# Kernel optimization log

Hardware: AMD Instinct MI355X
Metric: run time of the kernel (lower is better)

## Reference

```python
import jax, jax.numpy as jnp
import numpy as np

# ---- model constants (match init_kwargs) ----
NX, NY, H, K, GRID = 32, 1, 64, 3, 5
MID = 2 * H + 1            # 129, middle width of each KAN block
NB = GRID + K              # 8 B-spline basis functions per edge
BATCH = 65536


def _grid_pts():
    # uniform extended grid on [-1, 1] with K extra knots each side: GRID+2K+1 pts
    step = 2.0 / GRID
    return jnp.arange(-K, GRID + K + 1, dtype=jnp.float32) * step - 1.0


def bspline_basis(x):
    """Cox-de Boor B-spline bases. x: [B, I] -> [B, I, GRID+K]."""
    g = _grid_pts()[None, None, :]          # [1,1,P]
    xe = x[..., None]                       # [B,I,1]
    B0 = ((xe >= g[..., :-1]) & (xe < g[..., 1:])).astype(x.dtype)
    Bp = B0
    for p in range(1, K + 1):
        left = (xe - g[..., :-(p + 1)]) / (g[..., p:-1] - g[..., :-(p + 1)])
        right = (g[..., p + 1:] - xe) / (g[..., p + 1:] - g[..., 1:-p])
        Bp = left * Bp[..., :-1] + right * Bp[..., 1:]
    return Bp  # [B, I, NB]


def kan_layer(x, coef, sb, ss, bias):
    """pykan KANLayer: y_o = sum_i sb[i,o]*silu(x_i) + ss[i,o]*spline_io(x_i) + bias_o.
    x: [B,I]; coef: [I,O,NB]; sb, ss: [I,O]; bias: [O]."""
    bs = bspline_basis(x)                                   # [B,I,NB]
    spline = jnp.einsum('bip,iop->bo', bs, coef * ss[:, :, None])
    return jax.nn.silu(x) @ sb + spline + bias


def setup_inputs() -> dict:
    key = jax.random.key(0)
    ks = iter(jax.random.split(key, 40))

    def xavier(k, shape, fan_in, fan_out):
        gain = np.sqrt(2.0)  # relu gain, as in the torch module
        std = gain * np.sqrt(2.0 / (fan_in + fan_out))
        return (std * jax.random.normal(k, shape, dtype=jnp.float32))

    inp = {
        'x': jax.random.normal(next(ks), (BATCH, NX), dtype=jnp.float32),
        'W_in': xavier(next(ks), (NX, H), NX, H),
        'b_in': jnp.zeros((H,), jnp.float32),
        'W_out': xavier(next(ks), (H, NY), H, NY),
    }
    for l in range(2):  # num_hidden_layers KAN blocks, each = 2 KANLayers
        for tag, (din, dout) in [('a', (H, MID)), ('b', (MID, H))]:
            inp[f'coef{l}{tag}'] = xavier(next(ks), (din, dout, NB), din * NB, dout)
            inp[f'sb{l}{tag}'] = xavier(next(ks), (din, dout), din, dout)
            inp[f'ss{l}{tag}'] = jnp.ones((din, dout), jnp.float32)
            inp[f'bias{l}{tag}'] = jnp.zeros((dout,), jnp.float32)
    return inp


def reference(x, W_in, b_in, W_out,
              coef0a, sb0a, ss0a, bias0a, coef0b, sb0b, ss0b, bias0b,
              coef1a, sb1a, ss1a, bias1a, coef1b, sb1b, ss1b, bias1b):
    h = jax.nn.relu(x @ W_in + b_in)
    for (ca, sa, ta, ba, cb, sbb, tb, bb) in (
        (coef0a, sb0a, ss0a, bias0a, coef0b, sb0b, ss0b, bias0b),
        (coef1a, sb1a, ss1a, bias1a, coef1b, sb1b, ss1b, bias1b),
    ):
        h = kan_layer(h, ca, sa, ta, ba)   # H -> 2H+1
        h = kan_layer(h, cb, sbb, tb, bb)  # 2H+1 -> H
    return jax.nn.sigmoid(h @ W_out)       # [B, NY]
```

## Files before the change

kernel.cpp:

```cpp
#include <hip/hip_runtime.h>
#include <math.h>
#include <stdint.h>

#define BATCH 65536
#define TB 128

typedef __fp16   fp16x2  __attribute__((ext_vector_type(2)));
typedef _Float16 half8   __attribute__((ext_vector_type(8)));
typedef float    floatx16 __attribute__((ext_vector_type(16)));

#define SH 68
#define SM 130
#define HM_SLICE (32*SM + 64)

#define WIN 2048
#define KSA 36
#define KSB 74
#define WA (KSA*5*512)
#define WB (KSB*2*512)
#define WTOT (WIN + 2*(WA+WB))

__global__ void setup_weights(
    const float* __restrict__ W_in,
    const float* __restrict__ c0a, const float* __restrict__ sb0a, const float* __restrict__ ss0a,
    const float* __restrict__ c0b, const float* __restrict__ sb0b, const float* __restrict__ ss0b,
    const float* __restrict__ c1a, const float* __restrict__ sb1a, const float* __restrict__ ss1a,
    const float* __restrict__ c1b, const float* __restrict__ sb1b, const float* __restrict__ ss1b,
    _Float16* __restrict__ wt) {
  int idx = blockIdx.x * 256 + threadIdx.x;
  if (idx >= WTOT) return;
  float v = 0.0f;
  if (idx < WIN) {
    int ks = idx >> 10; int nt = (idx >> 9) & 1;
    int q = idx & 511;  int l = q >> 3;   int j = q & 7;
    int n = nt*32 + (l & 31);
    int k = ks*16 + (l >> 5)*8 + j;
    v = W_in[k*64 + n];
  } else {
    int e2   = idx - WIN;
    int pair = (e2 >= WA + WB) ? 1 : 0;
    int e    = e2 - pair * (WA + WB);
    if (e < WA) {
      const float* coef = pair ? c1a : c0a;
      const float* sb   = pair ? sb1a : sb0a;
      const float* ss   = pair ? ss1a : ss0a;
      int ks = e / 2560; int r = e - ks*2560;
      int nt = r >> 9;   int q = r & 511;
      int l  = q >> 3;   int j = q & 7;
      int n  = nt*32 + (l & 31);
      int k  = ks*16 + (l >> 5)*8 + j;
      if (n < 129) {
        if (k < 512) { int i = k >> 3, p = k & 7; v = ss[i*129+n] * coef[(i*129+n)*8 + p]; }
        else         { int i = k - 512; if (i < 64) v = sb[i*129+n]; }
      }
    } else {
      const float* coef = pair ? c1b : c0b;
      const float* sb   = pair ? sb1b : sb0b;
      const float* ss   = pair ? ss1b : ss0b;
      int eb = e - WA;
      int ks = eb >> 10; int r = eb & 1023;
      int nt = r >> 9;   int q = r & 511;
      int l  = q >> 3;   int j = q & 7;
      int n  = nt*32 + (l & 31);
      int k  = ks*16 + (l >> 5)*8 + j;
      if (k < 1032)      { int i = k >> 3, p = k & 7; v = ss[i*64+n] * coef[(i*64+n)*8 + p]; }
      else if (k >= 1040){ int s = k - 1040; if (s < 129) v = sb[s*64+n]; }
    }
  }
  wt[idx] = (_Float16)v;
}

__device__ __forceinline__ half8 feat8(float x) {
  float s  = fmaf(x, 2.5f, 5.5f);
  float mf = floorf(s);
  int   m  = (int)mf;
  float u  = s - mf;
  float t  = 1.0f - u;
  float u2 = u*u;
  float t2 = t*t;
  float w0 = t2 * (t * (1.0f/6.0f));
  float w3 = u2 * (u * (1.0f/6.0f));
  float w1 = fmaf(u2, fmaf(0.5f, u, -1.0f), 2.0f/3.0f);
  float w2 = fmaf(t2, fmaf(0.5f, t, -1.0f), 2.0f/3.0f);
  union { fp16x2 h2[2]; uint64_t u64; } P;
  P.h2[0] = __builtin_amdgcn_cvt_pkrtz(w0, w1);
  P.h2[1] = __builtin_amdgcn_cvt_pkrtz(w2, w3);
  uint64_t T = ((unsigned)m <= 10u) ? P.u64 : 0ull;
  int A = (m << 4) - 48;
  uint64_t L  = T << (A & 63);
  uint64_t R_ = T >> ((-A) & 63);
  uint64_t q0 = (A >= 0) ? ((A < 64) ? L : 0ull) : R_;
  uint64_t q1 = (A >= 64) ? L : ((A > 0) ? R_ : 0ull);
  union { uint64_t q[2]; half8 h; } R;
  R.q[0] = q0; R.q[1] = q1;
  return R.h;
}

__device__ __forceinline__ float extract_half(uint32_t w, int khs) {
  union { uint32_t u; _Float16 h[2]; } cv;
  cv.u = w >> khs;
  return (float)cv.h[0];
}

__device__ __forceinline__ float silu(float x) {
  return x * __builtin_amdgcn_rcpf(1.0f + __expf(-x));
}

template<int KSPL, int KSIL, int NT, int SIN, int O, int SOUT>
__device__ __forceinline__ void kan_layer(
    const _Float16* __restrict__ hinw, _Float16* __restrict__ houtw,
    const _Float16* __restrict__ wt, const float* __restrict__ bias, int lane) {
  constexpr int KTOT = KSPL + KSIL;
  constexpr int NG   = KSPL / 8;
  constexpr int KR   = KSPL - NG*8;
  static_assert(KR == 0 || KR == 1, "remainder must be 0/1");
  const int ln  = lane & 31;
  const int kh  = lane >> 5;
  const int khs = kh << 4;
  const half8* __restrict__ bp = (const half8*)wt + lane;
  floatx16 acc[NT];
  #pragma unroll
  for (int j = 0; j < NT; ++j)
    #pragma unroll
    for (int e = 0; e < 16; ++e) acc[j][e] = 0.0f;

  half8 B[2][NT];
  #pragma unroll
  for (int d = 0; d < 2; ++d)
    #pragma unroll
    for (int j = 0; j < NT; ++j) B[d][j] = bp[(d*NT + j)*64];

  union H8 { half8 h; uint32_t d[4]; };

  #pragma unroll 1
  for (int g = 0; g < NG; ++g) {
    H8 ha, hb;
    ha.h = *(const half8*)&hinw[ln*SIN + g*16];
    hb.h = *(const half8*)&hinw[ln*SIN + g*16 + 8];
    #pragma unroll
    for (int u = 0; u < 8; ++u) {
      uint32_t w = (u < 4) ? ha.d[u] : hb.d[u & 3];
      half8 A = feat8(extract_half(w, khs));
      #pragma unroll
      for (int j = 0; j < NT; ++j)
        acc[j] = __builtin_amdgcn_mfma_f32_32x32x16_f16(A, B[u & 1][j], acc[j], 0, 0, 0);
      #pragma unroll
      for (int j = 0; j < NT; ++j)
        B[u & 1][j] = bp[((g*8 + u + 2)*NT + j)*64];
    }
  }

  if (KR == 1) {
    constexpr int ks = NG*8;
    H8 hc;
    hc.h = *(const half8*)&hinw[ln*SIN + ks*2];
    half8 A = feat8(extract_half(hc.d[0], khs));
    #pragma unroll
    for (int j = 0; j < NT; ++j)
      acc[j] = __builtin_amdgcn_mfma_f32_32x32x16_f16(A, B[ks & 1][j], acc[j], 0, 0, 0);
    #pragma unroll
    for (int j = 0; j < NT; ++j)
      B[ks & 1][j] = bp[((ks + 2)*NT + j)*64];
  }

  #pragma unroll
  for (int sk = 0; sk < KSIL; ++sk) {
    const int ks = KSPL + sk;
    half8 h8 = *(const half8*)&hinw[ln*SIN + sk*16 + kh*8];
    union { fp16x2 h2[4]; half8 v; } Au;
    #pragma unroll
    for (int e = 0; e < 4; ++e) {
      float s0 = silu((float)h8[2*e]);
      float s1 = silu((float)h8[2*e + 1]);
      Au.h2[e] = __builtin_amdgcn_cvt_pkrtz(s0, s1);
    }
    #pragma unroll
    for (int j = 0; j < NT; ++j)
      acc[j] = __builtin_amdgcn_mfma_f32_32x32x16_f16(Au.v, B[ks & 1][j], acc[j], 0, 0, 0);
    const int nks = (ks + 2 < KTOT) ? (ks + 2) : (KTOT - 1);
    #pragma unroll
    for (int j = 0; j < NT; ++j)
      B[ks & 1][j] = bp[(nks*NT + j)*64];
  }

  #pragma unroll
  for (int j = 0; j < NT; ++j) {
    int col = j*32 + ln;
    if (col < O) {
      float bv = bias[col];
      #pragma unroll
      for (int r = 0; r < 16; ++r) {
        int row = (r & 3) + 8*(r >> 2) + 4*kh;
        houtw[row*SOUT + col] = (_Float16)(acc[j][r] + bv);
      }
    }
  }
}

extern "C" __global__ void __launch_bounds__(256, 2)
kan_forward(const float* __restrict__ x, const float* __restrict__ b_in,
            const float* __restrict__ W_out, const _Float16* __restrict__ wt,
            const float* __restrict__ bias0a, const float* __restrict__ bias0b,
            const float* __restrict__ bias1a, const float* __restrict__ bias1b,
            float* __restrict__ out) {
  __shared__ _Float16 hM[4][HM_SLICE];
  __shared__ _Float16 hH[4][32*SH];
  const int t    = threadIdx.x;
  const int wv   = t >> 6;
  const int lane = t & 63;
  const int ln   = lane & 31;
  const int kh   = lane >> 5;
  _Float16* hMw = hM[wv];
  _Float16* hHw = hH[wv];
  const int rbase = blockIdx.x * TB + wv * 32;

  hMw[32*SM + lane] = (_Float16)0.0f;
  if (lane < 32) hMw[lane*SM + 129] = (_Float16)0.0f;

  {
    const float* xr = &x[(rbase + ln)*32 + kh*8];
    float4 v0 = *(const float4*)&xr[0];
    float4 v1 = *(const float4*)&xr[4];
    float4 v2 = *(const float4*)&xr[16];
    float4 v3 = *(const float4*)&xr[20];
    union { fp16x2 h2[4]; half8 h8; } A0, A1;
    A0.h2[0] = __builtin_amdgcn_cvt_pkrtz(v0.x, v0.y);
    A0.h2[1] = __builtin_amdgcn_cvt_pkrtz(v0.z, v0.w);
    A0.h2[2] = __builtin_amdgcn_cvt_pkrtz(v1.x, v1.y);
    A0.h2[3] = __builtin_amdgcn_cvt_pkrtz(v1.z, v1.w);
    A1.h2[0] = __builtin_amdgcn_cvt_pkrtz(v2.x, v2.y);
    A1.h2[1] = __builtin_amdgcn_cvt_pkrtz(v2.z, v2.w);
    A1.h2[2] = __builtin_amdgcn_cvt_pkrtz(v3.x, v3.y);
    A1.h2[3] = __builtin_amdgcn_cvt_pkrtz(v3.z, v3.w);
    const half8* bp = (const half8*)wt + lane;
    #pragma unroll
    for (int nt = 0; nt < 2; ++nt) {
      floatx16 a;
      #pragma unroll
      for (int e = 0; e < 16; ++e) a[e] = 0.0f;
      a = __builtin_amdgcn_mfma_f32_32x32x16_f16(A0.h8, bp[nt*64],       a, 0, 0, 0);
      a = __builtin_amdgcn_mfma_f32_32x32x16_f16(A1.h8, bp[(2 + nt)*64], a, 0, 0, 0);
      int col = nt*32 + ln;
      float bv = b_in[col];
      #pragma unroll
      for (int r = 0; r < 16; ++r) {
        int row = (r & 3) + 8*(r >> 2) + 4*kh;
        hHw[row*SH + col] = (_Float16)fmaxf(a[r] + bv, 0.0f);
      }
    }
  }

  kan_layer<32,4,5,SH,129,SM>(hHw, hMw, wt + WIN,             bias0a, lane);
  kan_layer<65,9,2,SM, 64,SH>(hMw, hHw, wt + WIN + WA,        bias0b, lane);
  kan_layer<32,4,5,SH,129,SM>(hHw, hMw, wt + WIN + WA + WB,   bias1a, lane);
  kan_layer<65,9,2,SM, 64,SH>(hMw, hHw, wt + WIN + 2*WA + WB, bias1b, lane);

  {
    float s = 0.0f;
    #pragma unroll
    for (int j = 0; j < 32; ++j)
      s = fmaf((float)hHw[ln*SH + kh*32 + j], W_out[kh*32 + j], s);
    s += __shfl_down(s, 32);
    if (lane < 32)
      out[rbase + ln] = __builtin_amdgcn_rcpf(1.0f + __expf(-s));
  }
}

extern "C" void kernel_launch(void* const* d_in, const int* in_sizes, int n_in,
                              void* d_out, int out_size, void* d_ws, size_t ws_size,
                              hipStream_t stream) {
  const float* x     = (const float*)d_in[0];
  const float* W_in  = (const float*)d_in[1];
  const float* b_in  = (const float*)d_in[2];
  const float* W_out = (const float*)d_in[3];
  const float* c0a = (const float*)d_in[4];  const float* sb0a = (const float*)d_in[5];
  const float* ss0a= (const float*)d_in[6];  const float* bias0a=(const float*)d_in[7];
  const float* c0b = (const float*)d_in[8];  const float* sb0b = (const float*)d_in[9];
  const float* ss0b= (const float*)d_in[10]; const float* bias0b=(const float*)d_in[11];
  const float* c1a = (const float*)d_in[12]; const float* sb1a = (const float*)d_in[13];
  const float* ss1a= (const float*)d_in[14]; const float* bias1a=(const float*)d_in[15];
  const float* c1b = (const float*)d_in[16]; const float* sb1b = (const float*)d_in[17];
  const float* ss1b= (const float*)d_in[18]; const float* bias1b=(const float*)d_in[19];
  float*    out = (float*)d_out;
  _Float16* wt  = (_Float16*)d_ws;

  setup_weights<<<(WTOT + 255)/256, 256, 0, stream>>>(
      W_in, c0a, sb0a, ss0a, c0b, sb0b, ss0b,
      c1a, sb1a, ss1a, c1b, sb1b, ss1b, wt);

  kan_forward<<<BATCH/TB, 256, 0, stream>>>(
      x, b_in, W_out, wt, bias0a, bias0b, bias1a, bias1b, out);
}
```

Baseline: 155.0 us.

## Stage KAN weights into shared LDS via cooperative async DMA with triple buffering

Instead of every wave loading its own copy of the B-operand weights straight from global memory into registers, the four waves now cooperatively DMA each weight chunk into shared memory with global_load_lds, using a three-slot ring and barriers. This aims to cut redundant global/L2 traffic by a factor of the wave count and to hide load latency behind MFMA work. The staging buffer reuses the other layer's activation LDS region, which adds block-wide barriers per chunk and couples the waves' progress. Biases are also preloaded into registers up front.

```diff
diff --git a/kernel.cpp b/kernel.cpp
--- a/kernel.cpp
+++ b/kernel.cpp
@@ -6,6 +6,7 @@
 #define TB 128
 
 typedef __fp16   fp16x2  __attribute__((ext_vector_type(2)));
+typedef _Float16 half4   __attribute__((ext_vector_type(4)));
 typedef _Float16 half8   __attribute__((ext_vector_type(8)));
 typedef float    floatx16 __attribute__((ext_vector_type(16)));
 
@@ -70,6 +71,36 @@
   wt[idx] = (_Float16)v;
 }
 
+__device__ __forceinline__ void dma16(const void* g, void* l) {
+  __builtin_amdgcn_global_load_lds(
+      (const __attribute__((address_space(1))) void*)g,
+      (__attribute__((address_space(3))) void*)l,
+      16, 0, 0);
+}
+
+template<int NL>
+__device__ __forceinline__ void dma_chunk(const _Float16* gsrc, _Float16* ldst,
+                                          int lane, int wv) {
+  const char* g = (const char*)gsrc + lane*16;
+  char* l = (char*)ldst;
+  #pragma unroll
+  for (int L = 0; L < NL; ++L)
+    if ((L & 3) == wv) dma16(g + L*1024, l + L*1024);
+}
+
+template<int N>
+__device__ __forceinline__ void waitv() {
+  if constexpr (N == 0)      asm volatile("s_waitcnt vmcnt(0)" ::: "memory");
+  else if constexpr (N == 1) asm volatile("s_waitcnt vmcnt(1)" ::: "memory");
+  else                       asm volatile("s_waitcnt vmcnt(2)" ::: "memory");
+}
+
+__device__ __forceinline__ void bar() {
+  asm volatile("" ::: "memory");
+  __builtin_amdgcn_s_barrier();
+  asm volatile("" ::: "memory");
+}
+
 __device__ __forceinline__ half8 feat8(float x) {
   float s  = fmaf(x, 2.5f, 5.5f);
   float mf = floorf(s);
@@ -109,64 +140,69 @@
 template<int KSPL, int KSIL, int NT, int SIN, int O, int SOUT>
 __device__ __forceinline__ void kan_layer(
     const _Float16* __restrict__ hinw, _Float16* __restrict__ houtw,
-    const _Float16* __restrict__ wt, const float* __restrict__ bias, int lane) {
-  constexpr int KTOT = KSPL + KSIL;
-  constexpr int NG   = KSPL / 8;
-  constexpr int KR   = KSPL - NG*8;
-  static_assert(KR == 0 || KR == 1, "remainder must be 0/1");
+    _Float16* __restrict__ stg, const _Float16* __restrict__ wtl,
+    const float* __restrict__ bv, int lane, int wv) {
+  constexpr int CTOT = (KSPL + KSIL) / 2;
+  constexpr int NPS  = KSPL / 2;
+  constexpr int MIX  = KSPL & 1;
+  constexpr int NPSI = (KSIL - MIX) / 2;
+  constexpr int CH   = NT * 1024;
+  constexpr int NL   = NT * 2;
+  constexpr int W    = (NL >= 8) ? 2 : 1;
+  static_assert(NPS + MIX + NPSI == CTOT, "chunk accounting");
   const int ln  = lane & 31;
   const int kh  = lane >> 5;
   const int khs = kh << 4;
-  const half8* __restrict__ bp = (const half8*)wt + lane;
+
   floatx16 acc[NT];
   #pragma unroll
   for (int j = 0; j < NT; ++j)
     #pragma unroll
     for (int e = 0; e < 16; ++e) acc[j][e] = 0.0f;
 
-  half8 B[2][NT];
-  #pragma unroll
-  for (int d = 0; d < 2; ++d)
-    #pragma unroll
-    for (int j = 0; j < NT; ++j) B[d][j] = bp[(d*NT + j)*64];
-
-  union H8 { half8 h; uint32_t d[4]; };
+  dma_chunk<NL>(wtl,      stg,      lane, wv);
+  dma_chunk<NL>(wtl + CH, stg + CH, lane, wv);
 
   #pragma unroll 1
-  for (int g = 0; g < NG; ++g) {
-    H8 ha, hb;
-    ha.h = *(const half8*)&hinw[ln*SIN + g*16];
-    hb.h = *(const half8*)&hinw[ln*SIN + g*16 + 8];
-    #pragma unroll
-    for (int u = 0; u < 8; ++u) {
-      uint32_t w = (u < 4) ? ha.d[u] : hb.d[u & 3];
-      half8 A = feat8(extract_half(w, khs));
-      #pragma unroll
-      for (int j = 0; j < NT; ++j)
-        acc[j] = __builtin_amdgcn_mfma_f32_32x32x16_f16(A, B[u & 1][j], acc[j], 0, 0, 0);
-      #pragma unroll
-      for (int j = 0; j < NT; ++j)
-        B[u & 1][j] = bp[((g*8 + u + 2)*NT + j)*64];
-    }
-  }
-
-  if (KR == 1) {
-    constexpr int ks = NG*8;
-    H8 hc;
-    hc.h = *(const half8*)&hinw[ln*SIN + ks*2];
-    half8 A = feat8(extract_half(hc.d[0], khs));
+  for (int c = 0; c < NPS; ++c) {
+    waitv<W>();
+    bar();
+    dma_chunk<NL>(wtl + (c+2)*CH, stg + ((c+2)%3)*CH, lane, wv);
+    const half8* bp = (const half8*)(stg + (c%3)*CH) + lane;
+    half8 b0[NT], b1[NT];
+    #pragma unroll
+    for (int j = 0; j < NT; ++j) b0[j] = bp[j*64];
+    #pragma unroll
+    for (int j = 0; j < NT; ++j) b1[j] = bp[(NT + j)*64];
+    union { half4 v; uint32_t d[2]; } hq;
+    hq.v = *(const half4*)&hinw[ln*SIN + 4*c];
+    half8 A0 = feat8(extract_half(hq.d[0], khs));
+    half8 A1 = feat8(extract_half(hq.d[1], khs));
     #pragma unroll
     for (int j = 0; j < NT; ++j)
-      acc[j] = __builtin_amdgcn_mfma_f32_32x32x16_f16(A, B[ks & 1][j], acc[j], 0, 0, 0);
+      acc[j] = __builtin_amdgcn_mfma_f32_32x32x16_f16(A0, b0[j], acc[j], 0, 0, 0);
     #pragma unroll
     for (int j = 0; j < NT; ++j)
-      B[ks & 1][j] = bp[((ks + 2)*NT + j)*64];
-  }
-
-  #pragma unroll
-  for (int sk = 0; sk < KSIL; ++sk) {
-    const int ks = KSPL + sk;
-    half8 h8 = *(const half8*)&hinw[ln*SIN + sk*16 + kh*8];
+      acc[j] = __builtin_amdgcn_mfma_f32_32x32x16_f16(A1, b1[j], acc[j], 0, 0, 0);
+  }
+
+  if constexpr (MIX) {
+    constexpr int c = NPS;
+    waitv<W>();
+    bar();
+    if constexpr (c + 2 < CTOT)
+      dma_chunk<NL>(wtl + (c+2)*CH, stg + ((c+2)%3)*CH, lane, wv);
+    const half8* bp = (const half8*)(stg + (c%3)*CH) + lane;
+    half8 b0[NT], b1[NT];
+    #pragma unroll
+    for (int j = 0; j < NT; ++j) b0[j] = bp[j*64];
+    #pragma unroll
+    for (int j = 0; j < NT; ++j) b1[j] = bp[(NT + j)*64];
+    half8 A0 = feat8((float)hinw[ln*SIN + 2*(KSPL-1) + kh]);
+    #pragma unroll
+    for (int j = 0; j < NT; ++j)
+      acc[j] = __builtin_amdgcn_mfma_f32_32x32x16_f16(A0, b0[j], acc[j], 0, 0, 0);
+    half8 h8 = *(const half8*)&hinw[ln*SIN + kh*8];
     union { fp16x2 h2[4]; half8 v; } Au;
     #pragma unroll
     for (int e = 0; e < 4; ++e) {
@@ -176,22 +212,50 @@
     }
     #pragma unroll
     for (int j = 0; j < NT; ++j)
-      acc[j] = __builtin_amdgcn_mfma_f32_32x32x16_f16(Au.v, B[ks & 1][j], acc[j], 0, 0, 0);
-    const int nks = (ks + 2 < KTOT) ? (ks + 2) : (KTOT - 1);
-    #pragma unroll
-    for (int j = 0; j < NT; ++j)
-      B[ks & 1][j] = bp[(nks*NT + j)*64];
-  }
+      acc[j] = __builtin_amdgcn_mfma_f32_32x32x16_f16(Au.v, b1[j], acc[j], 0, 0, 0);
+  }
+
+  #pragma unroll
+  for (int i = 0; i < NPSI; ++i) {
+    const int c = NPS + MIX + i;
+    if (c == CTOT - 1) waitv<0>(); else waitv<W>();
+    bar();
+    if (c + 2 < CTOT)
+      dma_chunk<NL>(wtl + (c+2)*CH, stg + ((c+2)%3)*CH, lane, wv);
+    const half8* bp = (const half8*)(stg + (c%3)*CH) + lane;
+    half8 bb[2][NT];
+    #pragma unroll
+    for (int j = 0; j < NT; ++j) bb[0][j] = bp[j*64];
+    #pragma unroll
+    for (int j = 0; j < NT; ++j) bb[1][j] = bp[(NT + j)*64];
+    #pragma unroll
+    for (int kl = 0; kl < 2; ++kl) {
+      const int sk = MIX + 2*i + kl;
+      half8 h8 = *(const half8*)&hinw[ln*SIN + sk*16 + kh*8];
+      union { fp16x2 h2[4]; half8 v; } Au;
+      #pragma unroll
+      for (int e = 0; e < 4; ++e) {
+        float s0 = silu((float)h8[2*e]);
+        float s1 = silu((float)h8[2*e + 1]);
+        Au.h2[e] = __builtin_amdgcn_cvt_pkrtz(s0, s1);
+      }
+      #pragma unroll
+      for (int j = 0; j < NT; ++j)
+        acc[j] = __builtin_amdgcn_mfma_f32_32x32x16_f16(Au.v, bb[kl][j], acc[j], 0, 0, 0);
+    }
+  }
+
+  bar();
 
   #pragma unroll
   for (int j = 0; j < NT; ++j) {
     int col = j*32 + ln;
     if (col < O) {
-      float bv = bias[col];
+      float b = bv[j];
       #pragma unroll
       for (int r = 0; r < 16; ++r) {
         int row = (r & 3) + 8*(r >> 2) + 4*kh;
-        houtw[row*SOUT + col] = (_Float16)(acc[j][r] + bv);
+        houtw[row*SOUT + col] = (_Float16)(acc[j][r] + b);
       }
     }
   }
@@ -203,8 +267,8 @@
             const float* __restrict__ bias0a, const float* __restrict__ bias0b,
             const float* __restrict__ bias1a, const float* __restrict__ bias1b,
             float* __restrict__ out) {
-  __shared__ _Float16 hM[4][HM_SLICE];
-  __shared__ _Float16 hH[4][32*SH];
+  __shared__ __align__(16) _Float16 hM[4][HM_SLICE];
+  __shared__ __align__(16) _Float16 hH[4][32*SH];
   const int t    = threadIdx.x;
   const int wv   = t >> 6;
   const int lane = t & 63;
@@ -212,13 +276,30 @@
   const int kh   = lane >> 5;
   _Float16* hMw = hM[wv];
   _Float16* hHw = hH[wv];
+  _Float16* stM = &hM[0][0];
+  _Float16* stH = &hH[0][0];
   const int rbase = blockIdx.x * TB + wv * 32;
 
-  hMw[32*SM + lane] = (_Float16)0.0f;
-  if (lane < 32) hMw[lane*SM + 129] = (_Float16)0.0f;
+  if (wv == 3) {
+    hMw[32*SM + lane] = (_Float16)0.0f;
+    if (lane >= 20 && lane < 32) hMw[lane*SM + 129] = (_Float16)0.0f;
+  }
+
+  float bA0[5], bA1[5], bB0[2], bB1[2], bi[2];
+  #pragma unroll
+  for (int j = 0; j < 5; ++j) {
+    int col = j*32 + ln; int cc = (col < 129) ? col : 0;
+    bA0[j] = bias0a[cc]; bA1[j] = bias1a[cc];
+  }
+  #pragma unroll
+  for (int j = 0; j < 2; ++j) {
+    int col = j*32 + ln;
+    bB0[j] = bias0b[col]; bB1[j] = bias1b[col]; bi[j] = b_in[col];
+  }
 
   {
-    const float* xr = &x[(rbase + ln)*32 + kh*8];
+    dma_chunk<4>(wt, stM, lane, wv);
+    const float* xr = &x[(size_t)(rbase + ln)*32 + kh*8];
     float4 v0 = *(const float4*)&xr[0];
     float4 v1 = *(const float4*)&xr[4];
     float4 v2 = *(const float4*)&xr[16];
@@ -232,7 +313,9 @@
     A1.h2[1] = __builtin_amdgcn_cvt_pkrtz(v2.z, v2.w);
     A1.h2[2] = __builtin_amdgcn_cvt_pkrtz(v3.x, v3.y);
     A1.h2[3] = __builtin_amdgcn_cvt_pkrtz(v3.z, v3.w);
-    const half8* bp = (const half8*)wt + lane;
+    waitv<0>();
+    bar();
+    const half8* bp = (const half8*)stM + lane;
     #pragma unroll
     for (int nt = 0; nt < 2; ++nt) {
       floatx16 a;
@@ -241,7 +324,7 @@
       a = __builtin_amdgcn_mfma_f32_32x32x16_f16(A0.h8, bp[nt*64],       a, 0, 0, 0);
       a = __builtin_amdgcn_mfma_f32_32x32x16_f16(A1.h8, bp[(2 + nt)*64], a, 0, 0, 0);
       int col = nt*32 + ln;
-      float bv = b_in[col];
+      float bv = bi[nt];
       #pragma unroll
       for (int r = 0; r < 16; ++r) {
         int row = (r & 3) + 8*(r >> 2) + 4*kh;
@@ -249,11 +332,12 @@
       }
     }
   }
-
-  kan_layer<32,4,5,SH,129,SM>(hHw, hMw, wt + WIN,             bias0a, lane);
-  kan_layer<65,9,2,SM, 64,SH>(hMw, hHw, wt + WIN + WA,        bias0b, lane);
-  kan_layer<32,4,5,SH,129,SM>(hHw, hMw, wt + WIN + WA + WB,   bias1a, lane);
-  kan_layer<65,9,2,SM, 64,SH>(hMw, hHw, wt + WIN + 2*WA + WB, bias1b, lane);
+  bar();
+
+  kan_layer<32,4,5,SH,129,SM>(hHw, hMw, stM, wt + WIN,             bA0, lane, wv);
+  kan_layer<65,9,2,SM, 64,SH>(hMw, hHw, stH, wt + WIN + WA,        bB0, lane, wv);
+  kan_layer<32,4,5,SH,129,SM>(hHw, hMw, stM, wt + WIN + WA + WB,   bA1, lane, wv);
+  kan_layer<65,9,2,SM, 64,SH>(hMw, hHw, stH, wt + WIN + 2*WA + WB, bB1, lane, wv);
 
   {
     float s = 0.0f;
```

New measurement: 169.7 us. 1.09x slower.

## Switch KAN MFMA tiling from 32x32x16 to 16x16x32 with 16-row wave tiles

Applied to the files above, without the earlier changes.

Each wave now processes 16 batch rows instead of 32, using 16x16x32 fp16 MFMA instructions with a new packed weight layout (32-wide K steps, 16-wide N tiles). The block tile drops to 64 rows and launch bounds allow 4 blocks per CU, aiming for higher occupancy and fewer wasted padded columns. The wide layer-a path (9 N tiles) loads B fragments per step instead of double-buffering them, to limit register pressure. The weight setup kernel now writes 8 halves per thread. The risk is that each weight fragment is reused across only 16 rows, so weight traffic per row doubles.

```diff
diff --git a/kernel.cpp b/kernel.cpp
--- a/kernel.cpp
+++ b/kernel.cpp
@@ -3,21 +3,20 @@
 #include <stdint.h>
 
 #define BATCH 65536
-#define TB 128
+#define TB 64
 
 typedef __fp16   fp16x2  __attribute__((ext_vector_type(2)));
 typedef _Float16 half8   __attribute__((ext_vector_type(8)));
-typedef float    floatx16 __attribute__((ext_vector_type(16)));
+typedef float    floatx4 __attribute__((ext_vector_type(4)));
 
 #define SH 68
-#define SM 130
-#define HM_SLICE (32*SM + 64)
+#define SM 168
 
 #define WIN 2048
-#define KSA 36
-#define KSB 74
-#define WA (KSA*5*512)
-#define WB (KSB*2*512)
+#define KSA 18
+#define KSB 38
+#define WA (KSA*9*512)
+#define WB (KSB*4*512)
 #define WTOT (WIN + 2*(WA+WB))
 
 __global__ void setup_weights(
@@ -27,47 +26,71 @@
     const float* __restrict__ c1a, const float* __restrict__ sb1a, const float* __restrict__ ss1a,
     const float* __restrict__ c1b, const float* __restrict__ sb1b, const float* __restrict__ ss1b,
     _Float16* __restrict__ wt) {
-  int idx = blockIdx.x * 256 + threadIdx.x;
-  if (idx >= WTOT) return;
-  float v = 0.0f;
-  if (idx < WIN) {
-    int ks = idx >> 10; int nt = (idx >> 9) & 1;
-    int q = idx & 511;  int l = q >> 3;   int j = q & 7;
-    int n = nt*32 + (l & 31);
-    int k = ks*16 + (l >> 5)*8 + j;
-    v = W_in[k*64 + n];
+  int e = (blockIdx.x * 256 + threadIdx.x) * 8;
+  if (e >= WTOT) return;
+  float v[8];
+  #pragma unroll
+  for (int j = 0; j < 8; ++j) v[j] = 0.0f;
+
+  if (e < WIN) {
+    int nt = e >> 9;
+    int l  = (e >> 3) & 63;
+    int n  = nt*16 + (l & 15);
+    int kb = (l >> 4) * 8;
+    #pragma unroll
+    for (int j = 0; j < 8; ++j) v[j] = W_in[(kb + j)*64 + n];
   } else {
-    int e2   = idx - WIN;
+    int e2   = e - WIN;
     int pair = (e2 >= WA + WB) ? 1 : 0;
-    int e    = e2 - pair * (WA + WB);
-    if (e < WA) {
+    int e3   = e2 - pair * (WA + WB);
+    if (e3 < WA) {
       const float* coef = pair ? c1a : c0a;
       const float* sb   = pair ? sb1a : sb0a;
       const float* ss   = pair ? ss1a : ss0a;
-      int ks = e / 2560; int r = e - ks*2560;
-      int nt = r >> 9;   int q = r & 511;
-      int l  = q >> 3;   int j = q & 7;
-      int n  = nt*32 + (l & 31);
-      int k  = ks*16 + (l >> 5)*8 + j;
+      int ks = e3 / 4608; int r = e3 - ks*4608;
+      int nt = r >> 9;    int l = (r >> 3) & 63;
+      int n  = nt*16 + (l & 15);
+      int kb = ks*32 + (l >> 4)*8;
       if (n < 129) {
-        if (k < 512) { int i = k >> 3, p = k & 7; v = ss[i*129+n] * coef[(i*129+n)*8 + p]; }
-        else         { int i = k - 512; if (i < 64) v = sb[i*129+n]; }
+        if (kb < 512) {
+          int i = kb >> 3;
+          float s = ss[i*129 + n];
+          const float* cp = &coef[(i*129 + n)*8];
+          #pragma unroll
+          for (int j = 0; j < 8; ++j) v[j] = s * cp[j];
+        } else {
+          #pragma unroll
+          for (int j = 0; j < 8; ++j) v[j] = sb[(kb - 512 + j)*129 + n];
+        }
       }
     } else {
       const float* coef = pair ? c1b : c0b;
       const float* sb   = pair ? sb1b : sb0b;
       const float* ss   = pair ? ss1b : ss0b;
-      int eb = e - WA;
-      int ks = eb >> 10; int r = eb & 1023;
-      int nt = r >> 9;   int q = r & 511;
-      int l  = q >> 3;   int j = q & 7;
-      int n  = nt*32 + (l & 31);
-      int k  = ks*16 + (l >> 5)*8 + j;
-      if (k < 1032)      { int i = k >> 3, p = k & 7; v = ss[i*64+n] * coef[(i*64+n)*8 + p]; }
-      else if (k >= 1040){ int s = k - 1040; if (s < 129) v = sb[s*64+n]; }
-    }
-  }
-  wt[idx] = (_Float16)v;
+      int e4 = e3 - WA;
+      int ks = e4 >> 11;  int r = e4 & 2047;
+      int nt = r >> 9;    int l = (r >> 3) & 63;
+      int n  = nt*16 + (l & 15);
+      int kb = ks*32 + (l >> 4)*8;
+      if (kb < 1032) {
+        int i = kb >> 3;
+        float s = ss[i*64 + n];
+        const float* cp = &coef[(i*64 + n)*8];
+        #pragma unroll
+        for (int j = 0; j < 8; ++j) v[j] = s * cp[j];
+      } else if (kb >= 1056) {
+        #pragma unroll
+        for (int j = 0; j < 8; ++j) {
+          int si = kb - 1056 + j;
+          if (si < 129) v[j] = sb[si*64 + n];
+        }
+      }
+    }
+  }
+  half8 h;
+  #pragma unroll
+  for (int j = 0; j < 8; ++j) h[j] = (_Float16)v[j];
+  *(half8*)&wt[e] = h;
 }
 
 __device__ __forceinline__ half8 feat8(float x) {
@@ -96,173 +119,183 @@
   return R.h;
 }
 
-__device__ __forceinline__ float extract_half(uint32_t w, int khs) {
-  union { uint32_t u; _Float16 h[2]; } cv;
-  cv.u = w >> khs;
-  return (float)cv.h[0];
-}
-
 __device__ __forceinline__ float silu(float x) {
   return x * __builtin_amdgcn_rcpf(1.0f + __expf(-x));
 }
 
 template<int KSPL, int KSIL, int NT, int SIN, int O, int SOUT>
-__device__ __forceinline__ void kan_layer(
+__device__ __forceinline__ void kan_layer16(
     const _Float16* __restrict__ hinw, _Float16* __restrict__ houtw,
-    const _Float16* __restrict__ wt, const float* __restrict__ bias, int lane) {
+    const _Float16* __restrict__ wtl, const float* __restrict__ bias, int lane) {
   constexpr int KTOT = KSPL + KSIL;
   constexpr int NG   = KSPL / 8;
   constexpr int KR   = KSPL - NG*8;
   static_assert(KR == 0 || KR == 1, "remainder must be 0/1");
-  const int ln  = lane & 31;
-  const int kh  = lane >> 5;
-  const int khs = kh << 4;
-  const half8* __restrict__ bp = (const half8*)wt + lane;
-  floatx16 acc[NT];
+  const int ln16 = lane & 15;
+  const int kg   = lane >> 4;
+  const half8* __restrict__ bp = (const half8*)wtl + lane;
+  floatx4 acc[NT];
   #pragma unroll
   for (int j = 0; j < NT; ++j)
     #pragma unroll
-    for (int e = 0; e < 16; ++e) acc[j][e] = 0.0f;
-
-  half8 B[2][NT];
-  #pragma unroll
-  for (int d = 0; d < 2; ++d)
-    #pragma unroll
-    for (int j = 0; j < NT; ++j) B[d][j] = bp[(d*NT + j)*64];
-
-  union H8 { half8 h; uint32_t d[4]; };
-
-  #pragma unroll 1
-  for (int g = 0; g < NG; ++g) {
-    H8 ha, hb;
-    ha.h = *(const half8*)&hinw[ln*SIN + g*16];
-    hb.h = *(const half8*)&hinw[ln*SIN + g*16 + 8];
-    #pragma unroll
-    for (int u = 0; u < 8; ++u) {
-      uint32_t w = (u < 4) ? ha.d[u] : hb.d[u & 3];
-      half8 A = feat8(extract_half(w, khs));
-      #pragma unroll
-      for (int j = 0; j < NT; ++j)
-        acc[j] = __builtin_amdgcn_mfma_f32_32x32x16_f16(A, B[u & 1][j], acc[j], 0, 0, 0);
-      #pragma unroll
-      for (int j = 0; j < NT; ++j)
-        B[u & 1][j] = bp[((g*8 + u + 2)*NT + j)*64];
-    }
-  }
-
-  if (KR == 1) {
-    constexpr int ks = NG*8;
-    H8 hc;
-    hc.h = *(const half8*)&hinw[ln*SIN + ks*2];
-    half8 A = feat8(extract_half(hc.d[0], khs));
-    #pragma unroll
-    for (int j = 0; j < NT; ++j)
-      acc[j] = __builtin_amdgcn_mfma_f32_32x32x16_f16(A, B[ks & 1][j], acc[j], 0, 0, 0);
-    #pragma unroll
-    for (int j = 0; j < NT; ++j)
-      B[ks & 1][j] = bp[((ks + 2)*NT + j)*64];
-  }
-
-  #pragma unroll
-  for (int sk = 0; sk < KSIL; ++sk) {
-    const int ks = KSPL + sk;
-    half8 h8 = *(const half8*)&hinw[ln*SIN + sk*16 + kh*8];
-    union { fp16x2 h2[4]; half8 v; } Au;
-    #pragma unroll
-    for (int e = 0; e < 4; ++e) {
-      float s0 = silu((float)h8[2*e]);
-      float s1 = silu((float)h8[2*e + 1]);
-      Au.h2[e] = __builtin_amdgcn_cvt_pkrtz(s0, s1);
-    }
-    #pragma unroll
-    for (int j = 0; j < NT; ++j)
-      acc[j] = __builtin_amdgcn_mfma_f32_32x32x16_f16(Au.v, B[ks & 1][j], acc[j], 0, 0, 0);
-    const int nks = (ks + 2 < KTOT) ? (ks + 2) : (KTOT - 1);
-    #pragma unroll
-    for (int j = 0; j < NT; ++j)
-      B[ks & 1][j] = bp[(nks*NT + j)*64];
+    for (int el = 0; el < 4; ++el) acc[j][el] = 0.0f;
+
+  if constexpr (NT <= 4) {
+    half8 B[2][NT];
+    #pragma unroll
+    for (int d = 0; d < 2; ++d)
+      #pragma unroll
+      for (int j = 0; j < NT; ++j) B[d][j] = bp[(d*NT + j)*64];
+
+    #pragma unroll 1
+    for (int g = 0; g < NG; ++g) {
+      #pragma unroll
+      for (int u = 0; u < 8; ++u) {
+        const int ks = g*8 + u;
+        half8 A = feat8((float)hinw[ln16*SIN + ks*4 + kg]);
+        #pragma unroll
+        for (int j = 0; j < NT; ++j)
+          acc[j] = __builtin_amdgcn_mfma_f32_16x16x32_f16(A, B[u & 1][j], acc[j], 0, 0, 0);
+        #pragma unroll
+        for (int j = 0; j < NT; ++j)
+          B[u & 1][j] = bp[((ks + 2)*NT + j)*64];
+      }
+    }
+    if constexpr (KR == 1) {
+      constexpr int ks = NG*8;
+      half8 A = feat8((float)hinw[ln16*SIN + ks*4 + kg]);
+      #pragma unroll
+      for (int j = 0; j < NT; ++j)
+        acc[j] = __builtin_amdgcn_mfma_f32_16x16x32_f16(A, B[ks & 1][j], acc[j], 0, 0, 0);
+      #pragma unroll
+      for (int j = 0; j < NT; ++j)
+        B[ks & 1][j] = bp[((ks + 2)*NT + j)*64];
+    }
+    #pragma unroll
+    for (int sk = 0; sk < KSIL; ++sk) {
+      const int ks = KSPL + sk;
+      half8 h8 = *(const half8*)&hinw[ln16*SIN + sk*32 + kg*8];
+      union { fp16x2 h2[4]; half8 v; } Au;
+      #pragma unroll
+      for (int el = 0; el < 4; ++el) {
+        float s0 = silu((float)h8[2*el]);
+        float s1 = silu((float)h8[2*el + 1]);
+        Au.h2[el] = __builtin_amdgcn_cvt_pkrtz(s0, s1);
+      }
+      #pragma unroll
+      for (int j = 0; j < NT; ++j)
+        acc[j] = __builtin_amdgcn_mfma_f32_16x16x32_f16(Au.v, B[ks & 1][j], acc[j], 0, 0, 0);
+      const int nks = (ks + 2 < KTOT) ? (ks + 2) : (KTOT - 1);
+      #pragma unroll
+      for (int j = 0; j < NT; ++j)
+        B[ks & 1][j] = bp[(nks*NT + j)*64];
+    }
+  } else {
+    #pragma unroll 1
+    for (int g = 0; g < NG; ++g) {
+      #pragma unroll
+      for (int u = 0; u < 8; ++u) {
+        const int ks = g*8 + u;
+        half8 b[NT];
+        #pragma unroll
+        for (int j = 0; j < NT; ++j) b[j] = bp[(ks*NT + j)*64];
+        half8 A = feat8((float)hinw[ln16*SIN + ks*4 + kg]);
+        #pragma unroll
+        for (int j = 0; j < NT; ++j)
+          acc[j] = __builtin_amdgcn_mfma_f32_16x16x32_f16(A, b[j], acc[j], 0, 0, 0);
+      }
+    }
+    static_assert(KR == 0 || NT <= 4, "layer-a has no remainder");
+    #pragma unroll
+    for (int sk = 0; sk < KSIL; ++sk) {
+      const int ks = KSPL + sk;
+      half8 b[NT];
+      #pragma unroll
+      for (int j = 0; j < NT; ++j) b[j] = bp[(ks*NT + j)*64];
+      half8 h8 = *(const half8*)&hinw[ln16*SIN + sk*32 + kg*8];
+      union { fp16x2 h2[4]; half8 v; } Au;
+      #pragma unroll
+      for (int el = 0; el < 4; ++el) {
+        float s0 = silu((float)h8[2*el]);
+        float s1 = silu((float)h8[2*el + 1]);
+        Au.h2[el] = __builtin_amdgcn_cvt_pkrtz(s0, s1);
+      }
+      #pragma unroll
+      for (int j = 0; j < NT; ++j)
+        acc[j] = __builtin_amdgcn_mfma_f32_16x16x32_f16(Au.v, b[j], acc[j], 0, 0, 0);
+    }
   }
 
   #pragma unroll
   for (int j = 0; j < NT; ++j) {
-    int col = j*32 + ln;
+    int col = j*16 + ln16;
     if (col < O) {
       float bv = bias[col];
       #pragma unroll
-      for (int r = 0; r < 16; ++r) {
-        int row = (r & 3) + 8*(r >> 2) + 4*kh;
-        houtw[row*SOUT + col] = (_Float16)(acc[j][r] + bv);
-      }
-    }
-  }
-}
-
-extern "C" __global__ void __launch_bounds__(256, 2)
+      for (int r = 0; r < 4; ++r)
+        houtw[(kg*4 + r)*SOUT + col] = (_Float16)(acc[j][r] + bv);
+    }
+  }
+}
+
+extern "C" __global__ void __launch_bounds__(256, 4)
 kan_forward(const float* __restrict__ x, const float* __restrict__ b_in,
             const float* __restrict__ W_out, const _Float16* __restrict__ wt,
             const float* __restrict__ bias0a, const float* __restrict__ bias0b,
             const float* __restrict__ bias1a, const float* __restrict__ bias1b,
             float* __restrict__ out) {
-  __shared__ _Float16 hM[4][HM_SLICE];
-  __shared__ _Float16 hH[4][32*SH];
+  __shared__ _Float16 hM[4][16*SM];
+  __shared__ _Float16 hH[4][16*SH];
   const int t    = threadIdx.x;
   const int wv   = t >> 6;
   const int lane = t & 63;
-  const int ln   = lane & 31;
-  const int kh   = lane >> 5;
+  const int ln16 = lane & 15;
+  const int kg   = lane >> 4;
   _Float16* hMw = hM[wv];
   _Float16* hHw = hH[wv];
-  const int rbase = blockIdx.x * TB + wv * 32;
-
-  hMw[32*SM + lane] = (_Float16)0.0f;
-  if (lane < 32) hMw[lane*SM + 129] = (_Float16)0.0f;
+  const int rbase = blockIdx.x * TB + wv * 16;
+
+  #pragma unroll
+  for (int r = 0; r < 16; ++r) hMw[r*SM + 104 + lane] = (_Float16)0.0f;
 
   {
-    const float* xr = &x[(rbase + ln)*32 + kh*8];
+    const float* xr = &x[(size_t)(rbase + ln16)*32 + kg*8];
     float4 v0 = *(const float4*)&xr[0];
     float4 v1 = *(const float4*)&xr[4];
-    float4 v2 = *(const float4*)&xr[16];
-    float4 v3 = *(const float4*)&xr[20];
-    union { fp16x2 h2[4]; half8 h8; } A0, A1;
-    A0.h2[0] = __builtin_amdgcn_cvt_pkrtz(v0.x, v0.y);
-    A0.h2[1] = __builtin_amdgcn_cvt_pkrtz(v0.z, v0.w);
-    A0.h2[2] = __builtin_amdgcn_cvt_pkrtz(v1.x, v1.y);
-    A0.h2[3] = __builtin_amdgcn_cvt_pkrtz(v1.z, v1.w);
-    A1.h2[0] = __builtin_amdgcn_cvt_pkrtz(v2.x, v2.y);
-    A1.h2[1] = __builtin_amdgcn_cvt_pkrtz(v2.z, v2.w);
-    A1.h2[2] = __builtin_amdgcn_cvt_pkrtz(v3.x, v3.y);
-    A1.h2[3] = __builtin_amdgcn_cvt_pkrtz(v3.z, v3.w);
+    union { fp16x2 h2[4]; half8 h8; } A;
+    A.h2[0] = __builtin_amdgcn_cvt_pkrtz(v0.x, v0.y);
+    A.h2[1] = __builtin_amdgcn_cvt_pkrtz(v0.z, v0.w);
+    A.h2[2] = __builtin_amdgcn_cvt_pkrtz(v1.x, v1.y);
+    A.h2[3] = __builtin_amdgcn_cvt_pkrtz(v1.z, v1.w);
     const half8* bp = (const half8*)wt + lane;
     #pragma unroll
-    for (int nt = 0; nt < 2; ++nt) {
-      floatx16 a;
-      #pragma unroll
-      for (int e = 0; e < 16; ++e) a[e] = 0.0f;
-      a = __builtin_amdgcn_mfma_f32_32x32x16_f16(A0.h8, bp[nt*64],       a, 0, 0, 0);
-      a = __builtin_amdgcn_mfma_f32_32x32x16_f16(A1.h8, bp[(2 + nt)*64], a, 0, 0, 0);
-      int col = nt*32 + ln;
+    for (int nt = 0; nt < 4; ++nt) {
+      floatx4 a;
+      #pragma unroll
+      for (int el = 0; el < 4; ++el) a[el] = 0.0f;
+      a = __builtin_amdgcn_mfma_f32_16x16x32_f16(A.h8, bp[nt*64], a, 0, 0, 0);
+      int col = nt*16 + ln16;
       float bv = b_in[col];
       #pragma unroll
-      for (int r = 0; r < 16; ++r) {
-        int row = (r & 3) + 8*(r >> 2) + 4*kh;
-        hHw[row*SH + col] = (_Float16)fmaxf(a[r] + bv, 0.0f);
-      }
-    }
-  }
-
-  kan_layer<32,4,5,SH,129,SM>(hHw, hMw, wt + WIN,             bias0a, lane);
-  kan_layer<65,9,2,SM, 64,SH>(hMw, hHw, wt + WIN + WA,        bias0b, lane);
-  kan_layer<32,4,5,SH,129,SM>(hHw, hMw, wt + WIN + WA + WB,   bias1a, lane);
-  kan_layer<65,9,2,SM, 64,SH>(hMw, hHw, wt + WIN + 2*WA + WB, bias1b, lane);
+      for (int r = 0; r < 4; ++r)
+        hHw[(kg*4 + r)*SH + col] = (_Float16)fmaxf(a[r] + bv, 0.0f);
+    }
+  }
+
+  kan_layer16<16,2,9,SH,129,SM>(hHw, hMw, wt + WIN,             bias0a, lane);
+  kan_layer16<33,5,4,SM, 64,SH>(hMw, hHw, wt + WIN + WA,        bias0b, lane);
+  kan_layer16<16,2,9,SH,129,SM>(hHw, hMw, wt + WIN + WA + WB,   bias1a, lane);
+  kan_layer16<33,5,4,SM, 64,SH>(hMw, hHw, wt + WIN + 2*WA + WB, bias1b, lane);
 
   {
     float s = 0.0f;
     #pragma unroll
-    for (int j = 0; j < 32; ++j)
-      s = fmaf((float)hHw[ln*SH + kh*32 + j], W_out[kh*32 + j], s);
-    s += __shfl_down(s, 32);
-    if (lane < 32)
-      out[rbase + ln] = __builtin_amdgcn_rcpf(1.0f + __expf(-s));
+    for (int j = 0; j < 16; ++j)
+      s = fmaf((float)hHw[ln16*SH + kg*16 + j], W_out[kg*16 + j], s);
+    s += __shfl_xor(s, 16);
+    s += __shfl_xor(s, 32);
+    if (lane < 16)
+      out[rbase + ln16] = __builtin_amdgcn_rcpf(1.0f + __expf(-s));
   }
 }
 
@@ -284,7 +317,7 @@
   float*    out = (float*)d_out;
   _Float16* wt  = (_Float16*)d_ws;
 
-  setup_weights<<<(WTOT + 255)/256, 256, 0, stream>>>(
+  setup_weights<<<(WTOT/8 + 255)/256, 256, 0, stream>>>(
       W_in, c0a, sb0a, ss0a, c0b, sb0b, ss0b,
       c1a, sb1a, ss1a, c1b, sb1b, ss1b, wt);
 
```

New measurement: 175.7 us. 13.4% more time.

## Split each KAN layer's K dimension across wave pairs with LDS reduction

Applied to the files above, without the earlier changes.

Each 32-row tile is now handled by two waves that split the reduction (K) range of every KAN layer. Each wave computes partial MFMA accumulators over its half of the spline and SiLU steps, and the partials are exchanged through fp32 shared memory and summed. Rows per block drop from 128 to 64 and the occupancy hint rises from 2 to 3 blocks. This targets the latency of the long serial MFMA chain per wave, at the cost of extra LDS traffic, three block barriers per layer, and twice as many waves loading the same weights.

```diff
diff --git a/kernel.cpp b/kernel.cpp
--- a/kernel.cpp
+++ b/kernel.cpp
@@ -3,15 +3,15 @@
 #include <stdint.h>
 
 #define BATCH 65536
-#define TB 128
+#define TB 64
 
 typedef __fp16   fp16x2  __attribute__((ext_vector_type(2)));
+typedef _Float16 half4   __attribute__((ext_vector_type(4)));
 typedef _Float16 half8   __attribute__((ext_vector_type(8)));
 typedef float    floatx16 __attribute__((ext_vector_type(16)));
 
 #define SH 68
 #define SM 130
-#define HM_SLICE (32*SM + 64)
 
 #define WIN 2048
 #define KSA 36
@@ -106,66 +106,59 @@
   return x * __builtin_amdgcn_rcpf(1.0f + __expf(-x));
 }
 
-template<int KSPL, int KSIL, int NT, int SIN, int O, int SOUT>
-__device__ __forceinline__ void kan_layer(
-    const _Float16* __restrict__ hinw, _Float16* __restrict__ houtw,
-    const _Float16* __restrict__ wt, const float* __restrict__ bias, int lane) {
+template<int KS0, int NPAIR, int REM, int NSIL, int KSPL, int KSIL, int NT, int SIN>
+__device__ __forceinline__ void kan_half(
+    const _Float16* __restrict__ hinw, const _Float16* __restrict__ wtl,
+    floatx16 (&acc)[NT], int lane) {
   constexpr int KTOT = KSPL + KSIL;
-  constexpr int NG   = KSPL / 8;
-  constexpr int KR   = KSPL - NG*8;
-  static_assert(KR == 0 || KR == 1, "remainder must be 0/1");
   const int ln  = lane & 31;
   const int kh  = lane >> 5;
   const int khs = kh << 4;
-  const half8* __restrict__ bp = (const half8*)wt + lane;
-  floatx16 acc[NT];
+  const half8* __restrict__ bp = (const half8*)wtl + lane;
   #pragma unroll
   for (int j = 0; j < NT; ++j)
     #pragma unroll
     for (int e = 0; e < 16; ++e) acc[j][e] = 0.0f;
 
-  half8 B[2][NT];
+  half8 B0v[NT], B1v[NT];
   #pragma unroll
-  for (int d = 0; d < 2; ++d)
-    #pragma unroll
-    for (int j = 0; j < NT; ++j) B[d][j] = bp[(d*NT + j)*64];
-
-  union H8 { half8 h; uint32_t d[4]; };
+  for (int j = 0; j < NT; ++j) B0v[j] = bp[((KS0    )*NT + j)*64];
+  #pragma unroll
+  for (int j = 0; j < NT; ++j) B1v[j] = bp[((KS0 + 1)*NT + j)*64];
 
   #pragma unroll 1
-  for (int g = 0; g < NG; ++g) {
-    H8 ha, hb;
-    ha.h = *(const half8*)&hinw[ln*SIN + g*16];
-    hb.h = *(const half8*)&hinw[ln*SIN + g*16 + 8];
-    #pragma unroll
-    for (int u = 0; u < 8; ++u) {
-      uint32_t w = (u < 4) ? ha.d[u] : hb.d[u & 3];
-      half8 A = feat8(extract_half(w, khs));
-      #pragma unroll
-      for (int j = 0; j < NT; ++j)
-        acc[j] = __builtin_amdgcn_mfma_f32_32x32x16_f16(A, B[u & 1][j], acc[j], 0, 0, 0);
-      #pragma unroll
-      for (int j = 0; j < NT; ++j)
-        B[u & 1][j] = bp[((g*8 + u + 2)*NT + j)*64];
-    }
-  }
-
-  if (KR == 1) {
-    constexpr int ks = NG*8;
-    H8 hc;
-    hc.h = *(const half8*)&hinw[ln*SIN + ks*2];
-    half8 A = feat8(extract_half(hc.d[0], khs));
+  for (int c = 0; c < NPAIR; ++c) {
+    const int ks0 = KS0 + 2*c;
+    union { half4 v; uint32_t d[2]; } hq;
+    hq.v = *(const half4*)&hinw[ln*SIN + 2*ks0];
+    half8 A0 = feat8(extract_half(hq.d[0], khs));
+    half8 A1 = feat8(extract_half(hq.d[1], khs));
     #pragma unroll
     for (int j = 0; j < NT; ++j)
-      acc[j] = __builtin_amdgcn_mfma_f32_32x32x16_f16(A, B[ks & 1][j], acc[j], 0, 0, 0);
+      acc[j] = __builtin_amdgcn_mfma_f32_32x32x16_f16(A0, B0v[j], acc[j], 0, 0, 0);
+    #pragma unroll
+    for (int j = 0; j < NT; ++j) B0v[j] = bp[((ks0 + 2)*NT + j)*64];
     #pragma unroll
     for (int j = 0; j < NT; ++j)
-      B[ks & 1][j] = bp[((ks + 2)*NT + j)*64];
+      acc[j] = __builtin_amdgcn_mfma_f32_32x32x16_f16(A1, B1v[j], acc[j], 0, 0, 0);
+    #pragma unroll
+    for (int j = 0; j < NT; ++j) B1v[j] = bp[((ks0 + 3)*NT + j)*64];
+  }
+
+  if constexpr (REM) {
+    constexpr int ks = KS0 + 2*NPAIR;
+    uint32_t w = *(const uint32_t*)&hinw[ln*SIN + 2*ks];
+    half8 A = feat8(extract_half(w, khs));
+    #pragma unroll
+    for (int j = 0; j < NT; ++j)
+      acc[j] = __builtin_amdgcn_mfma_f32_32x32x16_f16(A, B0v[j], acc[j], 0, 0, 0);
+    #pragma unroll
+    for (int j = 0; j < NT; ++j) B0v[j] = bp[((ks + 2)*NT + j)*64];
   }
 
   #pragma unroll
-  for (int sk = 0; sk < KSIL; ++sk) {
-    const int ks = KSPL + sk;
+  for (int sk = 0; sk < NSIL; ++sk) {
+    const int ksl = KSPL + sk;
     half8 h8 = *(const half8*)&hinw[ln*SIN + sk*16 + kh*8];
     union { fp16x2 h2[4]; half8 v; } Au;
     #pragma unroll
@@ -174,51 +167,150 @@
       float s1 = silu((float)h8[2*e + 1]);
       Au.h2[e] = __builtin_amdgcn_cvt_pkrtz(s0, s1);
     }
-    #pragma unroll
-    for (int j = 0; j < NT; ++j)
-      acc[j] = __builtin_amdgcn_mfma_f32_32x32x16_f16(Au.v, B[ks & 1][j], acc[j], 0, 0, 0);
-    const int nks = (ks + 2 < KTOT) ? (ks + 2) : (KTOT - 1);
-    #pragma unroll
-    for (int j = 0; j < NT; ++j)
-      B[ks & 1][j] = bp[(nks*NT + j)*64];
-  }
-
-  #pragma unroll
-  for (int j = 0; j < NT; ++j) {
-    int col = j*32 + ln;
-    if (col < O) {
-      float bv = bias[col];
+    const int nks = (ksl + 2 < KTOT) ? (ksl + 2) : (KTOT - 1);
+    if (((ksl - KS0) & 1) == 0) {
+      #pragma unroll
+      for (int j = 0; j < NT; ++j)
+        acc[j] = __builtin_amdgcn_mfma_f32_32x32x16_f16(Au.v, B0v[j], acc[j], 0, 0, 0);
+      #pragma unroll
+      for (int j = 0; j < NT; ++j) B0v[j] = bp[(nks*NT + j)*64];
+    } else {
+      #pragma unroll
+      for (int j = 0; j < NT; ++j)
+        acc[j] = __builtin_amdgcn_mfma_f32_32x32x16_f16(Au.v, B1v[j], acc[j], 0, 0, 0);
+      #pragma unroll
+      for (int j = 0; j < NT; ++j) B1v[j] = bp[(nks*NT + j)*64];
+    }
+  }
+}
+
+template<int KSPL, int KSIL, int NT, int JS, int SIN, int O, int SF, int S16,
+         int N0, int K1, int N1, int R1, int S1, bool TAILZ>
+__device__ __forceinline__ void kan_layer_ks(
+    const _Float16* __restrict__ hinw, float* __restrict__ foutF,
+    _Float16* __restrict__ hout16, const _Float16* __restrict__ wtl,
+    const float* __restrict__ bias, int lane, int role) {
+  constexpr int NJ0 = JS;
+  constexpr int NJ1 = NT - JS;
+  constexpr int NJM = (NJ0 > NJ1) ? NJ0 : NJ1;
+  const int ln = lane & 31;
+  const int kh = lane >> 5;
+  floatx16 acc[NT];
+  if (role == 0) kan_half<0,  N0, 0,  0,  KSPL, KSIL, NT, SIN>(hinw, wtl, acc, lane);
+  else           kan_half<K1, N1, R1, S1, KSPL, KSIL, NT, SIN>(hinw, wtl, acc, lane);
+
+  if (role == 0) {
+    #pragma unroll
+    for (int jj = 0; jj < NJ1; ++jj) {
+      const int j = JS + jj;
+      int col = j*32 + ln;
+      if (col < O) {
+        #pragma unroll
+        for (int r = 0; r < 16; ++r) {
+          int row = (r & 3) + 8*(r >> 2) + 4*kh;
+          foutF[row*SF + col] = acc[j][r];
+        }
+      }
+    }
+  } else {
+    #pragma unroll
+    for (int jj = 0; jj < NJ0; ++jj) {
+      int col = jj*32 + ln;
       #pragma unroll
       for (int r = 0; r < 16; ++r) {
         int row = (r & 3) + 8*(r >> 2) + 4*kh;
-        houtw[row*SOUT + col] = (_Float16)(acc[j][r] + bv);
-      }
-    }
-  }
-}
-
-extern "C" __global__ void __launch_bounds__(256, 2)
+        foutF[row*SF + col] = acc[jj][r];
+      }
+    }
+  }
+  __syncthreads();
+
+  float pre[NJM][16];
+  if (role == 0) {
+    #pragma unroll
+    for (int jj = 0; jj < NJ0; ++jj) {
+      int col = jj*32 + ln;
+      #pragma unroll
+      for (int r = 0; r < 16; ++r) {
+        int row = (r & 3) + 8*(r >> 2) + 4*kh;
+        pre[jj][r] = foutF[row*SF + col];
+      }
+    }
+  } else {
+    #pragma unroll
+    for (int jj = 0; jj < NJ1; ++jj) {
+      const int j = JS + jj;
+      int col = j*32 + ln;
+      bool ok = (col < O);
+      #pragma unroll
+      for (int r = 0; r < 16; ++r) {
+        int row = (r & 3) + 8*(r >> 2) + 4*kh;
+        pre[jj][r] = ok ? foutF[row*SF + col] : 0.0f;
+      }
+    }
+  }
+  __syncthreads();
+
+  if (role == 0) {
+    #pragma unroll
+    for (int jj = 0; jj < NJ0; ++jj) {
+      int col = jj*32 + ln;
+      float bv = bias[col];
+      #pragma unroll
+      for (int r = 0; r < 16; ++r) {
+        int row = (r & 3) + 8*(r >> 2) + 4*kh;
+        hout16[row*S16 + col] = (_Float16)(pre[jj][r] + acc[jj][r] + bv);
+      }
+    }
+  } else {
+    #pragma unroll
+    for (int jj = 0; jj < NJ1; ++jj) {
+      const int j = JS + jj;
+      int col = j*32 + ln;
+      if (col < O) {
+        float bv = bias[col];
+        #pragma unroll
+        for (int r = 0; r < 16; ++r) {
+          int row = (r & 3) + 8*(r >> 2) + 4*kh;
+          hout16[row*S16 + col] = (_Float16)(pre[jj][r] + acc[j][r] + bv);
+        }
+      } else if (O == 129 && col == 129) {
+        #pragma unroll
+        for (int r = 0; r < 16; ++r) {
+          int row = (r & 3) + 8*(r >> 2) + 4*kh;
+          hout16[row*S16 + col] = (_Float16)0.0f;
+        }
+      }
+    }
+    if (TAILZ && lane < 16)
+      hout16[32*S16 + lane] = (_Float16)0.0f;
+  }
+  __syncthreads();
+}
+
+extern "C" __global__ void __launch_bounds__(256, 3)
 kan_forward(const float* __restrict__ x, const float* __restrict__ b_in,
             const float* __restrict__ W_out, const _Float16* __restrict__ wt,
             const float* __restrict__ bias0a, const float* __restrict__ bias0b,
             const float* __restrict__ bias1a, const float* __restrict__ bias1b,
             float* __restrict__ out) {
-  __shared__ _Float16 hM[4][HM_SLICE];
-  __shared__ _Float16 hH[4][32*SH];
+  __shared__ __align__(16) float hMf[2][32*SM];
+  __shared__ __align__(16) float hHf[2][32*SH];
   const int t    = threadIdx.x;
   const int wv   = t >> 6;
   const int lane = t & 63;
   const int ln   = lane & 31;
   const int kh   = lane >> 5;
-  _Float16* hMw = hM[wv];
-  _Float16* hHw = hH[wv];
-  const int rbase = blockIdx.x * TB + wv * 32;
-
-  hMw[32*SM + lane] = (_Float16)0.0f;
-  if (lane < 32) hMw[lane*SM + 129] = (_Float16)0.0f;
+  const int p    = wv >> 1;
+  const int role = wv & 1;
+  float*     hMfp = hMf[p];
+  float*     hHfp = hHf[p];
+  _Float16*  hM16 = (_Float16*)hMfp;
+  _Float16*  hH16 = (_Float16*)hHfp;
+  const int rbase = blockIdx.x * TB + p * 32;
 
   {
-    const float* xr = &x[(rbase + ln)*32 + kh*8];
+    const float* xr = &x[(size_t)(rbase + ln)*32 + kh*8];
     float4 v0 = *(const float4*)&xr[0];
     float4 v1 = *(const float4*)&xr[4];
     float4 v2 = *(const float4*)&xr[16];
@@ -233,36 +325,37 @@
     A1.h2[2] = __builtin_amdgcn_cvt_pkrtz(v3.x, v3.y);
     A1.h2[3] = __builtin_amdgcn_cvt_pkrtz(v3.z, v3.w);
     const half8* bp = (const half8*)wt + lane;
-    #pragma unroll
-    for (int nt = 0; nt < 2; ++nt) {
-      floatx16 a;
-      #pragma unroll
-      for (int e = 0; e < 16; ++e) a[e] = 0.0f;
-      a = __builtin_amdgcn_mfma_f32_32x32x16_f16(A0.h8, bp[nt*64],       a, 0, 0, 0);
-      a = __builtin_amdgcn_mfma_f32_32x32x16_f16(A1.h8, bp[(2 + nt)*64], a, 0, 0, 0);
-      int col = nt*32 + ln;
-      float bv = b_in[col];
-      #pragma unroll
-      for (int r = 0; r < 16; ++r) {
-        int row = (r & 3) + 8*(r >> 2) + 4*kh;
-        hHw[row*SH + col] = (_Float16)fmaxf(a[r] + bv, 0.0f);
-      }
-    }
-  }
-
-  kan_layer<32,4,5,SH,129,SM>(hHw, hMw, wt + WIN,             bias0a, lane);
-  kan_layer<65,9,2,SM, 64,SH>(hMw, hHw, wt + WIN + WA,        bias0b, lane);
-  kan_layer<32,4,5,SH,129,SM>(hHw, hMw, wt + WIN + WA + WB,   bias1a, lane);
-  kan_layer<65,9,2,SM, 64,SH>(hMw, hHw, wt + WIN + 2*WA + WB, bias1b, lane);
+    floatx16 a;
+    #pragma unroll
+    for (int e = 0; e < 16; ++e) a[e] = 0.0f;
+    a = __builtin_amdgcn_mfma_f32_32x32x16_f16(A0.h8, bp[role*64],       a, 0, 0, 0);
+    a = __builtin_amdgcn_mfma_f32_32x32x16_f16(A1.h8, bp[(2 + role)*64], a, 0, 0, 0);
+    int col = role*32 + ln;
+    float bv = b_in[col];
+    #pragma unroll
+    for (int r = 0; r < 16; ++r) {
+      int row = (r & 3) + 8*(r >> 2) + 4*kh;
+      hH16[row*SH + col] = (_Float16)fmaxf(a[r] + bv, 0.0f);
+    }
+  }
+  __syncthreads();
+
+  kan_layer_ks<32,4,5,3,SH,129,SM,SM,  9, 18, 7,0,4, true >(hH16, hMfp, hM16, wt + WIN,             bias0a, lane, role);
+  kan_layer_ks<65,9,2,1,SM, 64,SH,SH, 19, 38,13,1,9, false>(hM16, hHfp, hH16, wt + WIN + WA,        bias0b, lane, role);
+  kan_layer_ks<32,4,5,3,SH,129,SM,SM,  9, 18, 7,0,4, true >(hH16, hMfp, hM16, wt + WIN + WA + WB,   bias1a, lane, role);
+  kan_layer_ks<65,9,2,1,SM, 64,SH,SH, 19, 38,13,1,9, false>(hM16, hHfp, hH16, wt + WIN + 2*WA + WB, bias1b, lane, role);
 
   {
+    int rr    = (lane & 15) + role*16;
+    int chunk = lane >> 4;
     float s = 0.0f;
     #pragma unroll
-    for (int j = 0; j < 32; ++j)
-      s = fmaf((float)hHw[ln*SH + kh*32 + j], W_out[kh*32 + j], s);
-    s += __shfl_down(s, 32);
-    if (lane < 32)
-      out[rbase + ln] = __builtin_amdgcn_rcpf(1.0f + __expf(-s));
+    for (int j = 0; j < 16; ++j)
+      s = fmaf((float)hH16[rr*SH + chunk*16 + j], W_out[chunk*16 + j], s);
+    s += __shfl_xor(s, 16);
+    s += __shfl_xor(s, 32);
+    if (lane < 16)
+      out[rbase + rr] = __builtin_amdgcn_rcpf(1.0f + __expf(-s));
   }
 }
 
```

New measurement: 184.7 us. 1.19x slower.
